# Kernel tuning notes

Hardware: AMD Instinct MI355X
Metric: run time of the kernel (lower is better)

Reference implementation:

```python
import jax, jax.numpy as jnp
import numpy as np

B, D, Q, V, E, H, C = 32, 1000, 50, 50000, 384, 384, 10


def setup_inputs():
    key = jax.random.key(0)
    ks = jax.random.split(key, 12)
    docs_input = jax.random.randint(ks[0], (B, D), 1, V)
    docs_len = jax.random.randint(ks[1], (B,), D // 2, D + 1).at[0].set(D)
    querys_input = jax.random.randint(ks[2], (B, Q), 1, V)
    querys_len = jax.random.randint(ks[3], (B,), Q // 2, Q + 1).at[0].set(Q)
    candidates = jax.random.randint(ks[4], (B, C), 1, V)
    emb = jax.random.uniform(ks[5], (V, E), minval=-0.05, maxval=0.05)
    p = lambda k, s: jax.random.normal(k, s) * 0.05
    return {
        'docs_input': docs_input, 'docs_len': docs_len,
        'querys_input': querys_input, 'querys_len': querys_len,
        'candidates': candidates, 'emb': emb,
        'Wih_f': p(ks[6], (3 * H, E)), 'Whh_f': p(ks[7], (3 * H, H)),
        'bih_f': jnp.zeros((3 * H,)), 'bhh_f': jnp.zeros((3 * H,)),
        'Wih_b': p(ks[8], (3 * H, E)), 'Whh_b': p(ks[9], (3 * H, H)),
        'bih_b': jnp.zeros((3 * H,)), 'bhh_b': jnp.zeros((3 * H,)),
    }


def _gru_dir(x, lens, Wih, Whh, bih, bhh):
    # x: [B,T,E]. Packed-seq semantics: state frozen and output zeroed past lens.
    Bt, T, _ = x.shape
    xw = jnp.einsum('bte,ge->btg', x, Wih) + bih          # [B,T,3H] input projections
    valid = (jnp.arange(T)[None, :] < lens[:, None])      # [B,T]

    def step(h, inp):
        xw_t, v = inp                                     # [B,3H], [B,1]
        hw = h @ Whh.T + bhh
        xr, xz, xn = jnp.split(xw_t, 3, axis=-1)
        hr, hz, hn = jnp.split(hw, 3, axis=-1)
        r = jax.nn.sigmoid(xr + hr)
        z = jax.nn.sigmoid(xz + hz)
        n = jnp.tanh(xn + r * hn)
        h_new = (1.0 - z) * n + z * h
        h = jnp.where(v, h_new, h)
        return h, jnp.where(v, h_new, 0.0)

    h0 = jnp.zeros((Bt, Whh.shape[1]), x.dtype)
    _, outs = jax.lax.scan(step, h0, (xw.transpose(1, 0, 2), valid.T[:, :, None]))
    return outs.transpose(1, 0, 2)                        # [B,T,H]


def _bigru(x, lens, Wih_f, Whh_f, bih_f, bhh_f, Wih_b, Whh_b, bih_b, bhh_b):
    T = x.shape[1]
    t = jnp.arange(T)[None, :]
    # per-sequence reversal indices (identity on padded tail)
    ridx = jnp.where(t < lens[:, None], lens[:, None] - 1 - t, t)
    x_rev = jnp.take_along_axis(x, ridx[:, :, None], axis=1)
    out_f = _gru_dir(x, lens, Wih_f, Whh_f, bih_f, bhh_f)
    out_b = _gru_dir(x_rev, lens, Wih_b, Whh_b, bih_b, bhh_b)
    out_b = jnp.take_along_axis(out_b, ridx[:, :, None], axis=1)
    return jnp.concatenate([out_f, out_b], axis=-1)       # [B,T,2H]


def _softmax_mask(x, mask, axis, eps=1e-12):
    shift = jnp.max(x, axis=axis, keepdims=True)
    e = jnp.exp(x - shift) * mask
    return e / (jnp.sum(e, axis=axis, keepdims=True) + eps)


def reference(docs_input, docs_len, querys_input, querys_len, candidates, emb,
              Wih_f, Whh_f, bih_f, bhh_f, Wih_b, Whh_b, bih_b, bhh_b):
    gp = (Wih_f, Whh_f, bih_f, bhh_f, Wih_b, Whh_b, bih_b, bhh_b)
    dos = _bigru(emb[docs_input], docs_len, *gp)          # [B,D,2H]
    qos = _bigru(emb[querys_input], querys_len, *gp)      # [B,Q,2H]
    dmask = (jnp.arange(dos.shape[1])[None, :] < docs_len[:, None]).astype(dos.dtype)
    qmask = (jnp.arange(qos.shape[1])[None, :] < querys_len[:, None]).astype(qos.dtype)
    M = jnp.einsum('bdh,bqh->bdq', dos, qos)              # pairwise doc-query scores
    M_mask = dmask[:, :, None] * qmask[:, None, :]
    alpha = _softmax_mask(M, M_mask, axis=1)              # softmax over doc axis
    beta = _softmax_mask(M, M_mask, axis=2)               # softmax over query axis
    avg_beta = jnp.sum(beta, axis=1) / docs_len[:, None].astype(beta.dtype)  # [B,Q]
    s = jnp.einsum('bdq,bq->bd', alpha, avg_beta)         # attention-over-attention, [B,D]
    # per-candidate boolean-mask sum (vectorized segment reduce)
    pointer = (docs_input[:, None, :] == candidates[:, :, None]).astype(s.dtype)  # [B,C,D]
    pb = jnp.einsum('bcd,bd->bc', pointer, s)             # candidate scores
    return pb
```

## Files before the change

### kernel.cpp

```cpp
#include <hip/hip_runtime.h>
#include <math.h>

#define B_  32
#define D_  1000
#define Q_  50
#define E_  384
#define H_  384
#define G3_ 1152
#define C_  10
#define P_  192

typedef _Float16 f16;
typedef f16 f16x2 __attribute__((ext_vector_type(2)));

__global__ __launch_bounds__(256) void k_packw(const float* __restrict__ Wf,
                                               const float* __restrict__ Wb,
                                               f16x2* __restrict__ WTP) {
  int idx = blockIdx.x * 256 + threadIdx.x;
  if (idx >= 3 * P_ * H_) return;
  int g = idx / (P_ * H_);
  int rem = idx % (P_ * H_);
  int p = rem / H_, j = rem % H_;
  const float* W = blockIdx.y ? Wb : Wf;
  float a = W[(size_t)(g * H_ + j) * H_ + 2 * p];
  float b = W[(size_t)(g * H_ + j) * H_ + 2 * p + 1];
  WTP[(size_t)blockIdx.y * 3 * P_ * H_ + idx] = (f16x2){(f16)a, (f16)b};
}

__global__ __launch_bounds__(256) void k_projx(
    const int* __restrict__ toks, const int* __restrict__ lens, int T, int CT, int c,
    const float* __restrict__ emb,
    const float* __restrict__ Wih_f, const float* __restrict__ bih_f,
    const float* __restrict__ Wih_b, const float* __restrict__ bih_b,
    float* __restrict__ outbuf) {
  int dir = blockIdx.z;
  const float* W    = dir ? Wih_b : Wih_f;
  const float* bias = dir ? bih_b : bih_f;
  float* Cout = outbuf + (size_t)dir * B_ * CT * G3_;
  int nrows = B_ * CT;
  int r0 = blockIdx.x * 64, g0 = blockIdx.y * 64;
  int tid = threadIdx.x;

  const float* aRow[4];
  #pragma unroll
  for (int i = 0; i < 4; ++i) {
    int rr = (tid + 256 * i) >> 4;
    int row = r0 + rr; if (row >= nrows) row = nrows - 1;
    int b = row / CT, sl = row % CT;
    int s = c * CT + sl;
    int len = lens[b];
    int pos = dir ? (len - 1 - s) : s;
    if (pos < 0) pos = 0;
    if (pos >= T) pos = T - 1;
    aRow[i] = emb + (size_t)toks[b * T + pos] * E_;
  }

  __shared__ float As[64][17];
  __shared__ float Ws_[64][17];
  float acc[4][4] = {};
  for (int ec = 0; ec < E_; ec += 16) {
    #pragma unroll
    for (int i = 0; i < 4; ++i) {
      int lin = tid + 256 * i;
      int rr = lin >> 4, cc = lin & 15;
      As[rr][cc]  = aRow[i][ec + cc];
      Ws_[rr][cc] = W[(size_t)(g0 + rr) * E_ + ec + cc];
    }
    __syncthreads();
    int ty = tid >> 4, tx = tid & 15;
    #pragma unroll
    for (int kk = 0; kk < 16; ++kk) {
      float a[4], w[4];
      #pragma unroll
      for (int i = 0; i < 4; ++i) a[i] = As[ty + 16 * i][kk];
      #pragma unroll
      for (int j = 0; j < 4; ++j) w[j] = Ws_[tx + 16 * j][kk];
      #pragma unroll
      for (int i = 0; i < 4; ++i)
        #pragma unroll
        for (int j = 0; j < 4; ++j) acc[i][j] = fmaf(a[i], w[j], acc[i][j]);
    }
    __syncthreads();
  }
  int ty = tid >> 4, tx = tid & 15;
  #pragma unroll
  for (int i = 0; i < 4; ++i) {
    int row = r0 + ty + 16 * i;
    if (row < nrows) {
      #pragma unroll
      for (int j = 0; j < 4; ++j) {
        int g = g0 + tx + 16 * j;
        Cout[(size_t)row * G3_ + g] = acc[i][j] + bias[g];
      }
    }
  }
}

__global__ __launch_bounds__(384) void k_gruc(
    const float* __restrict__ xwC, int T, int CT, int c, int init,
    const f16x2* __restrict__ WTP,
    const float* __restrict__ bhhf, const float* __restrict__ bhhb,
    const int* __restrict__ lens,
    float* __restrict__ outbase, float* __restrict__ hcar) {
  int wg = blockIdx.x;
  int b = wg % B_, dir = wg / B_;
  int len = lens[b];
  int s0 = c * CT;
  int cnt = len - s0;
  if (cnt > CT) cnt = CT;
  if (cnt < 0) cnt = 0;
  const float* xw = xwC + (size_t)(dir * B_ + b) * CT * G3_;
  const f16x2* Wd = WTP + (size_t)dir * 3 * P_ * H_;
  const f16x2* wr = Wd;
  const f16x2* wz = Wd + (size_t)P_ * H_;
  const f16x2* wn = Wd + (size_t)2 * P_ * H_;
  const float* bhh = dir ? bhhb : bhhf;
  float* out = outbase + (size_t)b * T * 2 * H_ + dir * H_;
  float* hc = hcar + (size_t)(dir * B_ + b) * H_;

  int j = threadIdx.x;
  __shared__ f16x2 hs2[P_];
  f16* hs = (f16*)hs2;
  float hreg = init ? 0.f : hc[j];
  hs[j] = (f16)hreg;
  float br = bhh[j], bz = bhh[H_ + j], bn = bhh[2 * H_ + j];
  __syncthreads();

  for (int sl = 0; sl < cnt; ++sl) {
    int s = s0 + sl;
    int pos = dir ? (len - 1 - s) : s;
    const float* xp = xw + (size_t)sl * G3_;
    float hr = br, hz = bz, hn = bn;
    #pragma unroll 16
    for (int p = 0; p < P_; ++p) {
      f16x2 hp = hs2[p];
      f16x2 a = wr[p * H_ + j];
      f16x2 cc = wz[p * H_ + j];
      f16x2 d = wn[p * H_ + j];
#if __has_builtin(__builtin_amdgcn_fdot2)
      hr = __builtin_amdgcn_fdot2(a, hp, hr, false);
      hz = __builtin_amdgcn_fdot2(cc, hp, hz, false);
      hn = __builtin_amdgcn_fdot2(d, hp, hn, false);
#else
      hr = fmaf((float)a.x, (float)hp.x, hr); hr = fmaf((float)a.y, (float)hp.y, hr);
      hz = fmaf((float)cc.x, (float)hp.x, hz); hz = fmaf((float)cc.y, (float)hp.y, hz);
      hn = fmaf((float)d.x, (float)hp.x, hn); hn = fmaf((float)d.y, (float)hp.y, hn);
#endif
    }
    float r = 1.f / (1.f + expf(-(xp[j] + hr)));
    float z = 1.f / (1.f + expf(-(xp[H_ + j] + hz)));
    float n = tanhf(xp[2 * H_ + j] + r * hn);
    float hnew = (1.f - z) * n + z * hreg;
    __syncthreads();
    hs[j] = (f16)hnew;
    hreg = hnew;
    out[(size_t)pos * 2 * H_ + j] = hnew;
    __syncthreads();
  }
  hc[j] = hreg;
}

__global__ __launch_bounds__(256) void k_scores(const float* __restrict__ dos,
                                                const float* __restrict__ qos,
                                                const int* __restrict__ dlen,
                                                const int* __restrict__ qlen,
                                                float* __restrict__ M) {
  int b = blockIdx.x, d0 = blockIdx.y * 64;
  if (d0 >= dlen[b]) return;
  __shared__ float Ds[64][65];
  __shared__ float Qs[50][65];
  int tid = threadIdx.x;
  int lane = tid & 63, qg = tid >> 6;
  float acc[13];
  #pragma unroll
  for (int i = 0; i < 13; ++i) acc[i] = 0.f;
  for (int kc = 0; kc < 2 * H_; kc += 64) {
    #pragma unroll
    for (int i = 0; i < 16; ++i) {
      int lin = tid + 256 * i;
      int rr = lin >> 6, cc = lin & 63;
      int dd = d0 + rr; if (dd >= D_) dd = D_ - 1;
      Ds[rr][cc] = dos[((size_t)b * D_ + dd) * (2 * H_) + kc + cc];
    }
    #pragma unroll
    for (int i = 0; i < 13; ++i) {
      int lin = tid + 256 * i;
      if (lin < 3200) {
        int rr = lin >> 6, cc = lin & 63;
        Qs[rr][cc] = qos[((size_t)b * Q_ + rr) * (2 * H_) + kc + cc];
      }
    }
    __syncthreads();
    #pragma unroll 8
    for (int kk = 0; kk < 64; ++kk) {
      float dv = Ds[lane][kk];
      #pragma unroll
      for (int i = 0; i < 13; ++i) {
        int q = qg + 4 * i;
        if (q < 50) acc[i] = fmaf(dv, Qs[q][kk], acc[i]);
      }
    }
    __syncthreads();
  }
  if (d0 + lane < D_) {
    #pragma unroll
    for (int i = 0; i < 13; ++i) {
      int q = qg + 4 * i;
      if (q < 50) M[((size_t)b * D_ + d0 + lane) * 50 + q] = acc[i];
    }
  }
}

__global__ __launch_bounds__(256) void k_rowstats(const float* __restrict__ M,
                                                  const int* __restrict__ dlen,
                                                  const int* __restrict__ qlen,
                                                  float* __restrict__ rowmax,
                                                  float* __restrict__ rowsum) {
  int b = blockIdx.x;
  int d = blockIdx.y * 256 + threadIdx.x;
  if (d >= dlen[b]) return;
  int ql = qlen[b];
  const float* row = M + ((size_t)b * D_ + d) * 50;
  float m = 0.f;
  for (int q = 0; q < ql; ++q) m = fmaxf(m, row[q]);
  float s = 0.f;
  for (int q = 0; q < ql; ++q) s += expf(row[q] - m);
  rowmax[b * D_ + d] = m;
  rowsum[b * D_ + d] = s;
}

__global__ __launch_bounds__(256) void k_colstats(const float* __restrict__ M,
                                                  const int* __restrict__ dlen,
                                                  const int* __restrict__ qlen,
                                                  const float* __restrict__ rowmax,
                                                  const float* __restrict__ rowsum,
                                                  float* __restrict__ colmax,
                                                  float* __restrict__ colsum,
                                                  float* __restrict__ avg_beta) {
  int b = blockIdx.x, q = blockIdx.y;
  if (q >= qlen[b]) return;
  int dl = dlen[b];
  int tid = threadIdx.x;
  __shared__ float red[4];
  __shared__ float r1[4], r2[4];
  float m = 0.f;
  for (int d = tid; d < dl; d += 256) m = fmaxf(m, M[((size_t)b * D_ + d) * 50 + q]);
  for (int o = 32; o > 0; o >>= 1) m = fmaxf(m, __shfl_down(m, o, 64));
  if ((tid & 63) == 0) red[tid >> 6] = m;
  __syncthreads();
  m = fmaxf(fmaxf(red[0], red[1]), fmaxf(red[2], red[3]));
  float s1 = 0.f, s2 = 0.f;
  for (int d = tid; d < dl; d += 256) {
    float v = M[((size_t)b * D_ + d) * 50 + q];
    s1 += expf(v - m);
    s2 += expf(v - rowmax[b * D_ + d]) / (rowsum[b * D_ + d] + 1e-12f);
  }
  for (int o = 32; o > 0; o >>= 1) {
    s1 += __shfl_down(s1, o, 64);
    s2 += __shfl_down(s2, o, 64);
  }
  if ((tid & 63) == 0) { r1[tid >> 6] = s1; r2[tid >> 6] = s2; }
  __syncthreads();
  if (tid == 0) {
    colmax[b * 50 + q] = m;
    colsum[b * 50 + q] = r1[0] + r1[1] + r1[2] + r1[3];
    avg_beta[b * 50 + q] = (r2[0] + r2[1] + r2[2] + r2[3]) / (float)dl;
  }
}

__global__ __launch_bounds__(256) void k_svec(const float* __restrict__ M,
                                              const int* __restrict__ dlen,
                                              const int* __restrict__ qlen,
                                              const float* __restrict__ colmax,
                                              const float* __restrict__ colsum,
                                              const float* __restrict__ avg_beta,
                                              float* __restrict__ svec) {
  int b = blockIdx.x;
  int d = blockIdx.y * 256 + threadIdx.x;
  if (d >= dlen[b]) return;
  int ql = qlen[b];
  const float* row = M + ((size_t)b * D_ + d) * 50;
  float s = 0.f;
  for (int q = 0; q < ql; ++q)
    s += expf(row[q] - colmax[b * 50 + q]) / (colsum[b * 50 + q] + 1e-12f) * avg_beta[b * 50 + q];
  svec[b * D_ + d] = s;
}

__global__ __launch_bounds__(256) void k_pointer(const int* __restrict__ docs,
                                                 const int* __restrict__ cand,
                                                 const int* __restrict__ dlen,
                                                 const float* __restrict__ svec,
                                                 float* __restrict__ out) {
  int b = blockIdx.x, tid = threadIdx.x;
  __shared__ int cs[C_];
  __shared__ float accs[C_];
  if (tid < C_) { cs[tid] = cand[b * C_ + tid]; accs[tid] = 0.f; }
  __syncthreads();
  float loc[C_];
  #pragma unroll
  for (int c = 0; c < C_; ++c) loc[c] = 0.f;
  int dl = dlen[b];
  for (int d = tid; d < dl; d += 256) {
    int t = docs[b * D_ + d];
    float sv = svec[b * D_ + d];
    #pragma unroll
    for (int c = 0; c < C_; ++c)
      if (t == cs[c]) loc[c] += sv;
  }
  #pragma unroll
  for (int c = 0; c < C_; ++c)
    if (loc[c] != 0.f) atomicAdd(&accs[c], loc[c]);
  __syncthreads();
  if (tid < C_) out[b * C_ + tid] = accs[tid];
}

extern "C" void kernel_launch(void* const* d_in, const int* in_sizes, int n_in,
                              void* d_out, int out_size, void* d_ws, size_t ws_size,
                              hipStream_t stream) {
  const int* docs_input   = (const int*)d_in[0];
  const int* docs_len     = (const int*)d_in[1];
  const int* querys_input = (const int*)d_in[2];
  const int* querys_len   = (const int*)d_in[3];
  const int* candidates   = (const int*)d_in[4];
  const float* emb   = (const float*)d_in[5];
  const float* Wih_f = (const float*)d_in[6];
  const float* Whh_f = (const float*)d_in[7];
  const float* bih_f = (const float*)d_in[8];
  const float* bhh_f = (const float*)d_in[9];
  const float* Wih_b = (const float*)d_in[10];
  const float* Whh_b = (const float*)d_in[11];
  const float* bih_b = (const float*)d_in[12];
  const float* bhh_b = (const float*)d_in[13];
  float* out = (float*)d_out;

  float* ws = (float*)d_ws;
  size_t off = 0;
  auto alloc = [&](size_t n) { float* p = ws + off; off += n; return p; };

  f16x2* WTP   = (f16x2*)alloc((size_t)2 * 3 * P_ * H_);
  float* xwQ   = alloc((size_t)2 * B_ * Q_ * G3_);
  float* qcar  = alloc((size_t)2 * B_ * H_);
  float* dcar  = alloc((size_t)2 * B_ * H_);
  float* dos   = alloc((size_t)B_ * D_ * 2 * H_);
  float* qos   = alloc((size_t)B_ * Q_ * 2 * H_);
  float* Mm    = alloc((size_t)B_ * D_ * 50);
  float* rowmax = alloc((size_t)B_ * D_);
  float* rowsum = alloc((size_t)B_ * D_);
  float* colmax = alloc((size_t)B_ * 50);
  float* colsum = alloc((size_t)B_ * 50);
  float* avgb   = alloc((size_t)B_ * 50);
  float* svec   = alloc((size_t)B_ * D_);

  const int cts[8] = {1000, 500, 250, 125, 50, 25, 10, 5};
  int CT = 5;
  for (int i = 0; i < 8; ++i) {
    size_t need = (off + (size_t)2 * B_ * cts[i] * G3_) * sizeof(float);
    if (need <= ws_size) { CT = cts[i]; break; }
  }
  float* xwC = alloc((size_t)2 * B_ * CT * G3_);
  int NC = (D_ + CT - 1) / CT;

  k_packw<<<dim3((3 * P_ * H_ + 255) / 256, 2), 256, 0, stream>>>(Whh_f, Whh_b, WTP);

  k_projx<<<dim3((B_ * Q_ + 63) / 64, G3_ / 64, 2), 256, 0, stream>>>(
      querys_input, querys_len, Q_, Q_, 0, emb, Wih_f, bih_f, Wih_b, bih_b, xwQ);
  k_gruc<<<2 * B_, 384, 0, stream>>>(xwQ, Q_, Q_, 0, 1, WTP, bhh_f, bhh_b,
                                     querys_len, qos, qcar);

  for (int c = 0; c < NC; ++c) {
    k_projx<<<dim3((B_ * CT + 63) / 64, G3_ / 64, 2), 256, 0, stream>>>(
        docs_input, docs_len, D_, CT, c, emb, Wih_f, bih_f, Wih_b, bih_b, xwC);
    k_gruc<<<2 * B_, 384, 0, stream>>>(xwC, D_, CT, c, (c == 0) ? 1 : 0, WTP,
                                       bhh_f, bhh_b, docs_len, dos, dcar);
  }

  k_scores<<<dim3(B_, (D_ + 63) / 64), 256, 0, stream>>>(dos, qos, docs_len, querys_len, Mm);
  k_rowstats<<<dim3(B_, (D_ + 255) / 256), 256, 0, stream>>>(Mm, docs_len, querys_len, rowmax, rowsum);
  k_colstats<<<dim3(B_, 50), 256, 0, stream>>>(Mm, docs_len, querys_len, rowmax, rowsum,
                                               colmax, colsum, avgb);
  k_svec<<<dim3(B_, (D_ + 255) / 256), 256, 0, stream>>>(Mm, docs_len, querys_len,
                                                         colmax, colsum, avgb, svec);
  k_pointer<<<B_, 256, 0, stream>>>(docs_input, candidates, docs_len, svec, out);
}
```

Measured before the change: 10.80 ms.

## Split GRU recurrence across workgroups with LDS-resident weights and atomic grid barrier

The recurrent step is now split by hidden-unit slice across 24 workgroups per direction instead of one workgroup per batch and direction. Each workgroup keeps its fp16 slice of Whh in LDS, and all 32 batch rows are processed across the lanes. The shared hidden state is double-buffered in global memory, and a per-direction atomic counter acts as a grid barrier after each timestep. This removes the per-step re-streaming of the full recurrent weight matrix from L2 by every block, at the cost of one cross-workgroup barrier per step and a spin-wait that assumes all workgroups are co-resident. The input projection is also rewritten to use fp16 weights and embeddings held in LDS with packed dot2 accumulation.

After: 18.77 ms. 1.74x slower.

```diff
diff --git a/kernel.cpp b/kernel.cpp
--- a/kernel.cpp
+++ b/kernel.cpp
@@ -8,43 +8,58 @@
 #define H_  384
 #define G3_ 1152
 #define C_  10
-#define P_  192
+#define GD_ 24
+#define JW_ 16
 
 typedef _Float16 f16;
 typedef f16 f16x2 __attribute__((ext_vector_type(2)));
-
-__global__ __launch_bounds__(256) void k_packw(const float* __restrict__ Wf,
-                                               const float* __restrict__ Wb,
-                                               f16x2* __restrict__ WTP) {
-  int idx = blockIdx.x * 256 + threadIdx.x;
-  if (idx >= 3 * P_ * H_) return;
-  int g = idx / (P_ * H_);
-  int rem = idx % (P_ * H_);
-  int p = rem / H_, j = rem % H_;
-  const float* W = blockIdx.y ? Wb : Wf;
-  float a = W[(size_t)(g * H_ + j) * H_ + 2 * p];
-  float b = W[(size_t)(g * H_ + j) * H_ + 2 * p + 1];
-  WTP[(size_t)blockIdx.y * 3 * P_ * H_ + idx] = (f16x2){(f16)a, (f16)b};
-}
-
-__global__ __launch_bounds__(256) void k_projx(
+typedef f16 f16x4 __attribute__((ext_vector_type(4)));
+
+__device__ __forceinline__ float dot2f(f16x2 a, f16x2 b, float c) {
+#if __has_builtin(__builtin_amdgcn_fdot2)
+  return __builtin_amdgcn_fdot2(a, b, c, false);
+#else
+  return fmaf((float)a.x, (float)b.x, fmaf((float)a.y, (float)b.y, c));
+#endif
+}
+__device__ __forceinline__ f16x2 bc2(unsigned u) { return __builtin_bit_cast(f16x2, u); }
+
+__global__ __launch_bounds__(256) void k_packw2(const float* __restrict__ a0,
+                                                const float* __restrict__ a1,
+                                                const float* __restrict__ a2,
+                                                const float* __restrict__ a3,
+                                                f16* __restrict__ WQhh,
+                                                f16* __restrict__ WQih) {
+  const int n4 = G3_ * H_ / 4;
+  int i = blockIdx.x * 256 + threadIdx.x;
+  if (i >= n4) return;
+  int y = blockIdx.y;
+  const float* src = (y == 0) ? a0 : (y == 1) ? a1 : (y == 2) ? a2 : a3;
+  f16* dst = (y < 2) ? (WQhh + (size_t)y * G3_ * H_) : (WQih + (size_t)(y - 2) * G3_ * H_);
+  float4 v = *(const float4*)(src + (size_t)i * 4);
+  f16x4 o; o[0] = (f16)v.x; o[1] = (f16)v.y; o[2] = (f16)v.z; o[3] = (f16)v.w;
+  *(f16x4*)(dst + (size_t)i * 4) = o;
+}
+
+__global__ __launch_bounds__(256) void k_projx2(
     const int* __restrict__ toks, const int* __restrict__ lens, int T, int CT, int c,
-    const float* __restrict__ emb,
-    const float* __restrict__ Wih_f, const float* __restrict__ bih_f,
-    const float* __restrict__ Wih_b, const float* __restrict__ bih_b,
+    const float* __restrict__ emb, const f16* __restrict__ WQih,
+    const float* __restrict__ bih_f, const float* __restrict__ bih_b,
     float* __restrict__ outbuf) {
-  int dir = blockIdx.z;
-  const float* W    = dir ? Wih_b : Wih_f;
+  int dir = blockIdx.y;
+  const f16* W = WQih + (size_t)dir * G3_ * E_;
   const float* bias = dir ? bih_b : bih_f;
   float* Cout = outbuf + (size_t)dir * B_ * CT * G3_;
   int nrows = B_ * CT;
-  int r0 = blockIdx.x * 64, g0 = blockIdx.y * 64;
+  int r0 = blockIdx.x * 64;
   int tid = threadIdx.x;
 
-  const float* aRow[4];
-  #pragma unroll
-  for (int i = 0; i < 4; ++i) {
-    int rr = (tid + 256 * i) >> 4;
+  __shared__ f16 Als[64][386];
+  __shared__ f16 Wls[16][386];
+
+  for (int it = 0; it < 48; ++it) {
+    int slot = tid + 256 * it;
+    int rr = slot / 192, pp = slot % 192;
     int row = r0 + rr; if (row >= nrows) row = nrows - 1;
     int b = row / CT, sl = row % CT;
     int s = c * CT + sl;
@@ -52,112 +67,200 @@
     int pos = dir ? (len - 1 - s) : s;
     if (pos < 0) pos = 0;
     if (pos >= T) pos = T - 1;
-    aRow[i] = emb + (size_t)toks[b * T + pos] * E_;
-  }
-
-  __shared__ float As[64][17];
-  __shared__ float Ws_[64][17];
-  float acc[4][4] = {};
-  for (int ec = 0; ec < E_; ec += 16) {
-    #pragma unroll
-    for (int i = 0; i < 4; ++i) {
-      int lin = tid + 256 * i;
-      int rr = lin >> 4, cc = lin & 15;
-      As[rr][cc]  = aRow[i][ec + cc];
-      Ws_[rr][cc] = W[(size_t)(g0 + rr) * E_ + ec + cc];
-    }
-    __syncthreads();
-    int ty = tid >> 4, tx = tid & 15;
-    #pragma unroll
-    for (int kk = 0; kk < 16; ++kk) {
-      float a[4], w[4];
+    const float2 v = *(const float2*)(emb + (size_t)toks[b * T + pos] * E_ + pp * 2);
+    f16x2 h2; h2[0] = (f16)v.x; h2[1] = (f16)v.y;
+    *(f16x2*)&Als[rr][pp * 2] = h2;
+  }
+
+  int r2 = tid >> 3;
+  int g2 = tid & 7;
+
+  for (int g0 = 0; g0 < G3_; g0 += 16) {
+    __syncthreads();
+    for (int it = 0; it < 12; ++it) {
+      int slot = tid + 256 * it;
+      int rr = slot / 192, pp = slot % 192;
+      unsigned u = *(const unsigned*)(W + (size_t)(g0 + rr) * E_ + pp * 2);
+      *(unsigned*)&Wls[rr][pp * 2] = u;
+    }
+    __syncthreads();
+
+    float acc[2][2] = {};
+    for (int kb = 0; kb < 192; kb += 8) {
+      f16x2 a[2][8], w[2][8];
       #pragma unroll
-      for (int i = 0; i < 4; ++i) a[i] = As[ty + 16 * i][kk];
+      for (int kk = 0; kk < 8; ++kk) {
+        a[0][kk] = *(const f16x2*)&Als[r2 * 2    ][(kb + kk) * 2];
+        a[1][kk] = *(const f16x2*)&Als[r2 * 2 + 1][(kb + kk) * 2];
+        w[0][kk] = *(const f16x2*)&Wls[g2 * 2    ][(kb + kk) * 2];
+        w[1][kk] = *(const f16x2*)&Wls[g2 * 2 + 1][(kb + kk) * 2];
+      }
       #pragma unroll
-      for (int j = 0; j < 4; ++j) w[j] = Ws_[tx + 16 * j][kk];
-      #pragma unroll
-      for (int i = 0; i < 4; ++i)
-        #pragma unroll
-        for (int j = 0; j < 4; ++j) acc[i][j] = fmaf(a[i], w[j], acc[i][j]);
-    }
-    __syncthreads();
-  }
-  int ty = tid >> 4, tx = tid & 15;
-  #pragma unroll
-  for (int i = 0; i < 4; ++i) {
-    int row = r0 + ty + 16 * i;
-    if (row < nrows) {
-      #pragma unroll
-      for (int j = 0; j < 4; ++j) {
-        int g = g0 + tx + 16 * j;
-        Cout[(size_t)row * G3_ + g] = acc[i][j] + bias[g];
-      }
-    }
-  }
-}
-
-__global__ __launch_bounds__(384) void k_gruc(
-    const float* __restrict__ xwC, int T, int CT, int c, int init,
-    const f16x2* __restrict__ WTP,
+      for (int kk = 0; kk < 8; ++kk) {
+        acc[0][0] = dot2f(a[0][kk], w[0][kk], acc[0][0]);
+        acc[0][1] = dot2f(a[0][kk], w[1][kk], acc[0][1]);
+        acc[1][0] = dot2f(a[1][kk], w[0][kk], acc[1][0]);
+        acc[1][1] = dot2f(a[1][kk], w[1][kk], acc[1][1]);
+      }
+    }
+
+    #pragma unroll
+    for (int i = 0; i < 2; ++i) {
+      int row = r0 + r2 * 2 + i;
+      if (row < nrows) {
+        int g = g0 + g2 * 2;
+        float2 o = {acc[i][0] + bias[g], acc[i][1] + bias[g + 1]};
+        *(float2*)(Cout + (size_t)row * G3_ + g) = o;
+      }
+    }
+  }
+}
+
+__global__ __launch_bounds__(256) void k_grup(
+    const float* __restrict__ xw, int CTloc, int T, int s0, int cnt, int init,
+    const f16* __restrict__ WQhh,
     const float* __restrict__ bhhf, const float* __restrict__ bhhb,
     const int* __restrict__ lens,
-    float* __restrict__ outbase, float* __restrict__ hcar) {
-  int wg = blockIdx.x;
-  int b = wg % B_, dir = wg / B_;
+    f16* __restrict__ hglob, float* __restrict__ hcarF,
+    float* __restrict__ outbase, int* __restrict__ ctr) {
+  int dir = blockIdx.x / GD_;
+  int wgi = blockIdx.x % GD_;
+  int j0 = wgi * JW_;
+  int tid = threadIdx.x;
+  int wv = tid >> 6;
+  int lane = tid & 63;
+  int b = lane >> 1, ih = lane & 1;
+  int jbase = j0 + wv * 4;
   int len = lens[b];
-  int s0 = c * CT;
-  int cnt = len - s0;
-  if (cnt > CT) cnt = CT;
-  if (cnt < 0) cnt = 0;
-  const float* xw = xwC + (size_t)(dir * B_ + b) * CT * G3_;
-  const f16x2* Wd = WTP + (size_t)dir * 3 * P_ * H_;
-  const f16x2* wr = Wd;
-  const f16x2* wz = Wd + (size_t)P_ * H_;
-  const f16x2* wn = Wd + (size_t)2 * P_ * H_;
   const float* bhh = dir ? bhhb : bhhf;
-  float* out = outbase + (size_t)b * T * 2 * H_ + dir * H_;
-  float* hc = hcar + (size_t)(dir * B_ + b) * H_;
-
-  int j = threadIdx.x;
-  __shared__ f16x2 hs2[P_];
-  f16* hs = (f16*)hs2;
-  float hreg = init ? 0.f : hc[j];
-  hs[j] = (f16)hreg;
-  float br = bhh[j], bz = bhh[H_ + j], bn = bhh[2 * H_ + j];
+
+  __shared__ __align__(16) f16 wlds[3 * JW_ * H_];
+  __shared__ int sbail;
+  #pragma unroll
+  for (int it = 0; it < 9; ++it) {
+    int slot = tid + 256 * it;
+    int r = slot / 48, cc = slot % 48;
+    int g = r >> 4, jl = r & 15;
+    const f16* src = WQhh + ((size_t)dir * G3_ + g * H_ + j0 + jl) * H_ + cc * 8;
+    *(uint4*)&wlds[(size_t)r * H_ + cc * 8] = *(const uint4*)src;
+  }
+  if (tid == 0) sbail = 0;
+
+  float bj[3][4];
+  #pragma unroll
+  for (int g = 0; g < 3; ++g)
+    #pragma unroll
+    for (int jj = 0; jj < 4; ++jj) bj[g][jj] = bhh[g * H_ + jbase + jj];
+
+  float hold[4];
+  #pragma unroll
+  for (int jj = 0; jj < 4; ++jj)
+    hold[jj] = init ? 0.f : hcarF[((size_t)dir * B_ + b) * H_ + jbase + jj];
+
+  f16* h0 = hglob + ((size_t)dir * B_ + b) * H_;
+  float* outp = outbase + (size_t)b * T * 2 * H_ + dir * H_;
+  const float* xwb = xw + ((size_t)dir * B_ + b) * CTloc * G3_;
   __syncthreads();
+
+  float4 xwv[3];
+  if (ih == 0 && cnt > 0 && s0 < len) {
+    const float* xp = xwb;
+    #pragma unroll
+    for (int g = 0; g < 3; ++g) xwv[g] = *(const float4*)(xp + g * H_ + jbase);
+  }
 
   for (int sl = 0; sl < cnt; ++sl) {
     int s = s0 + sl;
+    bool alive = (s < len);
     int pos = dir ? (len - 1 - s) : s;
-    const float* xp = xw + (size_t)sl * G3_;
-    float hr = br, hz = bz, hn = bn;
-    #pragma unroll 16
-    for (int p = 0; p < P_; ++p) {
-      f16x2 hp = hs2[p];
-      f16x2 a = wr[p * H_ + j];
-      f16x2 cc = wz[p * H_ + j];
-      f16x2 d = wn[p * H_ + j];
-#if __has_builtin(__builtin_amdgcn_fdot2)
-      hr = __builtin_amdgcn_fdot2(a, hp, hr, false);
-      hz = __builtin_amdgcn_fdot2(cc, hp, hz, false);
-      hn = __builtin_amdgcn_fdot2(d, hp, hn, false);
-#else
-      hr = fmaf((float)a.x, (float)hp.x, hr); hr = fmaf((float)a.y, (float)hp.y, hr);
-      hz = fmaf((float)cc.x, (float)hp.x, hz); hz = fmaf((float)cc.y, (float)hp.y, hz);
-      hn = fmaf((float)d.x, (float)hp.x, hn); hn = fmaf((float)d.y, (float)hp.y, hn);
-#endif
-    }
-    float r = 1.f / (1.f + expf(-(xp[j] + hr)));
-    float z = 1.f / (1.f + expf(-(xp[H_ + j] + hz)));
-    float n = tanhf(xp[2 * H_ + j] + r * hn);
-    float hnew = (1.f - z) * n + z * hreg;
-    __syncthreads();
-    hs[j] = (f16)hnew;
-    hreg = hnew;
-    out[(size_t)pos * 2 * H_ + j] = hnew;
-    __syncthreads();
-  }
-  hc[j] = hreg;
+    bool hz = (init && sl == 0);
+    int rp = (s0 + sl) & 1;
+
+    uint4 hv[24];
+    if (!hz) {
+      const f16* hsrc = h0 + (size_t)rp * 2 * B_ * H_ + ih * 192;
+      #pragma unroll
+      for (int cc = 0; cc < 24; ++cc) hv[cc] = *(const uint4*)(hsrc + cc * 8);
+    }
+
+    float accs[3][4];
+    #pragma unroll
+    for (int g = 0; g < 3; ++g) {
+      #pragma unroll
+      for (int jj = 0; jj < 4; ++jj) {
+        float acc = 0.f;
+        if (!hz) {
+          const uint4* wp = (const uint4*)&wlds[(size_t)(g * JW_ + wv * 4 + jj) * H_ + ih * 192];
+          #pragma unroll
+          for (int cc = 0; cc < 24; ++cc) {
+            uint4 w4 = wp[cc];
+            acc = dot2f(bc2(w4.x), bc2(hv[cc].x), acc);
+            acc = dot2f(bc2(w4.y), bc2(hv[cc].y), acc);
+            acc = dot2f(bc2(w4.z), bc2(hv[cc].z), acc);
+            acc = dot2f(bc2(w4.w), bc2(hv[cc].w), acc);
+          }
+        }
+        float oth = __shfl_xor(acc, 1, 64);
+        accs[g][jj] = acc + oth;
+      }
+    }
+
+    if (ih == 0) {
+      if (alive) {
+        float xq[3][4];
+        #pragma unroll
+        for (int g = 0; g < 3; ++g) {
+          xq[g][0] = xwv[g].x; xq[g][1] = xwv[g].y; xq[g][2] = xwv[g].z; xq[g][3] = xwv[g].w;
+        }
+        #pragma unroll
+        for (int jj = 0; jj < 4; ++jj) {
+          float r = 1.f / (1.f + expf(-(xq[0][jj] + bj[0][jj] + accs[0][jj])));
+          float z = 1.f / (1.f + expf(-(xq[1][jj] + bj[1][jj] + accs[1][jj])));
+          float n = tanhf(xq[2][jj] + r * (bj[2][jj] + accs[2][jj]));
+          hold[jj] = (1.f - z) * n + z * hold[jj];
+        }
+        float4 o4 = {hold[0], hold[1], hold[2], hold[3]};
+        *(float4*)(outp + (size_t)pos * 2 * H_ + jbase) = o4;
+      }
+      f16x4 h16; h16[0] = (f16)hold[0]; h16[1] = (f16)hold[1];
+      h16[2] = (f16)hold[2]; h16[3] = (f16)hold[3];
+      *(f16x4*)(h0 + (size_t)(rp ^ 1) * 2 * B_ * H_ + jbase) = h16;
+
+      if (sl + 1 < cnt && s + 1 < len) {
+        const float* xp = xwb + (size_t)(sl + 1) * G3_;
+        #pragma unroll
+        for (int g = 0; g < 3; ++g) xwv[g] = *(const float4*)(xp + g * H_ + jbase);
+      }
+    }
+
+    __threadfence();
+    __syncthreads();
+    if (tid == 0) {
+      __hip_atomic_fetch_add(&ctr[dir], 1, __ATOMIC_RELEASE, __HIP_MEMORY_SCOPE_AGENT);
+      if (!sbail) {
+        int tgt = GD_ * (sl + 1);
+        int ok = 0;
+        for (int k = 0; k < 64; ++k) {
+          if (__hip_atomic_load(&ctr[dir], __ATOMIC_RELAXED, __HIP_MEMORY_SCOPE_AGENT) >= tgt) { ok = 1; break; }
+        }
+        if (!ok) {
+          long itc = 0;
+          while (__hip_atomic_load(&ctr[dir], __ATOMIC_RELAXED, __HIP_MEMORY_SCOPE_AGENT) < tgt) {
+            __builtin_amdgcn_s_sleep(1);
+            if (++itc > 5000000L) { sbail = 1; break; }
+          }
+        }
+      }
+    }
+    __syncthreads();
+    __threadfence();
+  }
+
+  if (ih == 0) {
+    #pragma unroll
+    for (int jj = 0; jj < 4; ++jj)
+      hcarF[((size_t)dir * B_ + b) * H_ + jbase + jj] = hold[jj];
+  }
 }
 
 __global__ __launch_bounds__(256) void k_scores(const float* __restrict__ dos,
@@ -337,13 +440,17 @@
   size_t off = 0;
   auto alloc = [&](size_t n) { float* p = ws + off; off += n; return p; };
 
-  f16x2* WTP   = (f16x2*)alloc((size_t)2 * 3 * P_ * H_);
-  float* xwQ   = alloc((size_t)2 * B_ * Q_ * G3_);
-  float* qcar  = alloc((size_t)2 * B_ * H_);
-  float* dcar  = alloc((size_t)2 * B_ * H_);
-  float* dos   = alloc((size_t)B_ * D_ * 2 * H_);
-  float* qos   = alloc((size_t)B_ * Q_ * 2 * H_);
-  float* Mm    = alloc((size_t)B_ * D_ * 50);
+  f16* WQhh = (f16*)alloc((size_t)G3_ * H_);
+  f16* WQih = (f16*)alloc((size_t)G3_ * H_);
+  f16* hgD  = (f16*)alloc((size_t)2 * B_ * H_);
+  f16* hgQ  = (f16*)alloc((size_t)2 * B_ * H_);
+  float* hcD = alloc((size_t)2 * B_ * H_);
+  float* hcQ = alloc((size_t)2 * B_ * H_);
+  int* ctr = (int*)alloc(16);
+  float* xwQ = alloc((size_t)2 * B_ * Q_ * G3_);
+  float* qos = alloc((size_t)B_ * Q_ * 2 * H_);
+  float* dos = alloc((size_t)B_ * D_ * 2 * H_);
+  float* Mm  = alloc((size_t)B_ * D_ * 50);
   float* rowmax = alloc((size_t)B_ * D_);
   float* rowsum = alloc((size_t)B_ * D_);
   float* colmax = alloc((size_t)B_ * 50);
@@ -357,21 +464,26 @@
     size_t need = (off + (size_t)2 * B_ * cts[i] * G3_) * sizeof(float);
     if (need <= ws_size) { CT = cts[i]; break; }
   }
-  float* xwC = alloc((size_t)2 * B_ * CT * G3_);
+  float* xwD = alloc((size_t)2 * B_ * CT * G3_);
   int NC = (D_ + CT - 1) / CT;
 
-  k_packw<<<dim3((3 * P_ * H_ + 255) / 256, 2), 256, 0, stream>>>(Whh_f, Whh_b, WTP);
-
-  k_projx<<<dim3((B_ * Q_ + 63) / 64, G3_ / 64, 2), 256, 0, stream>>>(
-      querys_input, querys_len, Q_, Q_, 0, emb, Wih_f, bih_f, Wih_b, bih_b, xwQ);
-  k_gruc<<<2 * B_, 384, 0, stream>>>(xwQ, Q_, Q_, 0, 1, WTP, bhh_f, bhh_b,
-                                     querys_len, qos, qcar);
+  hipMemsetAsync(ctr, 0, 64, stream);
+  k_packw2<<<dim3((G3_ * H_ / 4 + 255) / 256, 4), 256, 0, stream>>>(
+      Whh_f, Whh_b, Wih_f, Wih_b, WQhh, WQih);
+
+  k_projx2<<<dim3(B_ * Q_ / 64, 2), 256, 0, stream>>>(
+      querys_input, querys_len, Q_, Q_, 0, emb, WQih, bih_f, bih_b, xwQ);
+  k_grup<<<2 * GD_, 256, 0, stream>>>(xwQ, Q_, Q_, 0, Q_, 1, WQhh, bhh_f, bhh_b,
+                                      querys_len, hgQ, hcQ, qos, ctr + 2);
 
   for (int c = 0; c < NC; ++c) {
-    k_projx<<<dim3((B_ * CT + 63) / 64, G3_ / 64, 2), 256, 0, stream>>>(
-        docs_input, docs_len, D_, CT, c, emb, Wih_f, bih_f, Wih_b, bih_b, xwC);
-    k_gruc<<<2 * B_, 384, 0, stream>>>(xwC, D_, CT, c, (c == 0) ? 1 : 0, WTP,
-                                       bhh_f, bhh_b, docs_len, dos, dcar);
+    int s0 = c * CT;
+    int cntC = D_ - s0; if (cntC > CT) cntC = CT;
+    k_projx2<<<dim3(B_ * CT / 64, 2), 256, 0, stream>>>(
+        docs_input, docs_len, D_, CT, c, emb, WQih, bih_f, bih_b, xwD);
+    if (c > 0) hipMemsetAsync(ctr, 0, 8, stream);
+    k_grup<<<2 * GD_, 256, 0, stream>>>(xwD, CT, D_, s0, cntC, (c == 0) ? 1 : 0,
+                                        WQhh, bhh_f, bhh_b, docs_len, hgD, hcD, dos, ctr);
   }
 
   k_scores<<<dim3(B_, (D_ + 63) / 64), 256, 0, stream>>>(dos, qos, docs_len, querys_len, Mm);
```
